# Kernel optimization log

Measured on AMD Instinct MI355X. Metric: run time of the kernel, lower is better.

## Reference

```python
import jax, jax.numpy as jnp
import numpy as np

D_MODEL = 1024
NUM_HEADS = 16
DEPTH = D_MODEL // NUM_HEADS
B, S = 2, 2048


def setup_inputs() -> dict:
    key = jax.random.key(0)
    k1, k2, k3 = jax.random.split(key, 3)
    x = jax.random.normal(k1, (B, S, D_MODEL), dtype=jnp.float32)
    # causal mask: 1.0 where attention is disallowed (upper triangle)
    causal = 1.0 - jnp.tril(jnp.ones((S, S), dtype=jnp.float32))
    mask = causal[None, None, :, :]  # [1,1,S,S]
    w_attn = jax.random.normal(k2, (D_MODEL, 3 * D_MODEL), dtype=jnp.float32) * 0.02
    b_attn = jnp.zeros((3 * D_MODEL,), dtype=jnp.float32)
    w_proj = jax.random.normal(k3, (D_MODEL, D_MODEL), dtype=jnp.float32) * 0.02
    b_proj = jnp.zeros((D_MODEL,), dtype=jnp.float32)
    return {"x": x, "mask": mask, "w_attn": w_attn, "b_attn": b_attn,
            "w_proj": w_proj, "b_proj": b_proj}


def _split_heads(t):
    # [B,S,D] -> [B,H,S,depth]
    b, s, _ = t.shape
    return t.reshape(b, s, NUM_HEADS, DEPTH).transpose(0, 2, 1, 3)


def reference(x, mask, w_attn, b_attn, w_proj, b_proj):
    # QKV projection (Conv1d == pointwise dense over last axis)
    qkv = jnp.einsum('bsd,de->bse', x, w_attn) + b_attn
    q, k, v = jnp.split(qkv, 3, axis=2)
    q, k, v = _split_heads(q), _split_heads(k), _split_heads(v)  # [B,H,S,depth]
    present = jnp.stack([k, v], axis=1)  # [B,2,H,S,depth]
    # scaled dot-product attention (inference: no dropout)
    scores = jnp.einsum('bhqd,bhkd->bhqk', q, k) / jnp.sqrt(
        jnp.asarray(DEPTH, dtype=x.dtype))
    scores = scores + mask * (-1e9)
    attn = jax.nn.softmax(scores, axis=-1)
    out = jnp.einsum('bhqk,bhkd->bhqd', attn, v)
    # merge heads: [B,H,S,depth] -> [B,S,D]
    out = out.transpose(0, 2, 1, 3).reshape(x.shape[0], -1, D_MODEL)
    out = jnp.einsum('bsd,de->bse', out, w_proj) + b_proj
    return out, present
```

## Files before the change

### kernel.cpp

```cpp
#include <hip/hip_runtime.h>
#include <stdint.h>

typedef unsigned short u16;
typedef unsigned int u32;
typedef short bf16x8 __attribute__((ext_vector_type(8)));
typedef float f32x4 __attribute__((ext_vector_type(4)));

#define SEQ 2048
#define NH 16
#define DM 1024
#define DEPTH 64

#define QSCALE 0.18033688f
#define SMAX 16.0f

__device__ __forceinline__ u16 f2bf(float f) {
  union { float f; u32 i; } v; v.f = f;
  u32 x = v.i;
  x += 0x7fffu + ((x >> 16) & 1u);
  return (u16)(x >> 16);
}

__device__ __forceinline__ float fexp2(float x) {
#if __has_builtin(__builtin_amdgcn_exp2f)
  return __builtin_amdgcn_exp2f(x);
#else
  return exp2f(x);
#endif
}

__device__ __forceinline__ void gload_lds16(const u16* g, u16* l) {
  __builtin_amdgcn_global_load_lds(
      (const __attribute__((address_space(1))) u32*)g,
      (__attribute__((address_space(3))) u32*)l, 16, 0, 0);
}

__global__ __launch_bounds__(256)
void cvt_bf16(const float* __restrict__ src, u16* __restrict__ dst) {
  int i = (blockIdx.x * 256 + threadIdx.x) * 4;
  float4 v = *(const float4*)(src + i);
  ushort4 o; o.x = f2bf(v.x); o.y = f2bf(v.y); o.z = f2bf(v.z); o.w = f2bf(v.w);
  *(ushort4*)(dst + i) = o;
}

__global__ __launch_bounds__(256)
void cvtT_both(const float* __restrict__ wa, const float* __restrict__ wp,
               u16* __restrict__ dwa, u16* __restrict__ dwp) {
  __shared__ float t[32][33];
  const int tid = threadIdx.x;
  const int bx = blockIdx.x;
  const float* src; u16* dst; int N, n0;
  if (bx < 96) { src = wa; dst = dwa; N = 3 * DM; n0 = bx << 5; }
  else         { src = wp; dst = dwp; N = DM;     n0 = (bx - 96) << 5; }
  const int k0 = blockIdx.y << 5;
  const int K = DM;
  {
    int r = tid >> 3, c4 = (tid & 7) << 2;
    float4 v = *(const float4*)(src + (size_t)(k0 + r) * N + n0 + c4);
    t[r][c4 + 0] = v.x; t[r][c4 + 1] = v.y; t[r][c4 + 2] = v.z; t[r][c4 + 3] = v.w;
  }
  __syncthreads();
  {
    int n = tid >> 3, k4 = (tid & 7) << 2;
    ushort4 o;
    o.x = f2bf(t[k4 + 0][n]); o.y = f2bf(t[k4 + 1][n]);
    o.z = f2bf(t[k4 + 2][n]); o.w = f2bf(t[k4 + 3][n]);
    *(ushort4*)(dst + (size_t)(n0 + n) * K + k0 + k4) = o;
  }
}

__global__ __launch_bounds__(256)
void v_transpose(const float* __restrict__ present, u16* __restrict__ vt) {
  __shared__ float t[64][65];
  const int tid = threadIdx.x;
  const int st = blockIdx.x, bh = blockIdx.y;
  const int b = bh >> 4, h = bh & 15;
  const int s0 = st << 6;
  const float* vsrc = present + (((size_t)((b * 2 + 1) * NH + h)) * SEQ + s0) * DEPTH;
  u16* vdst = vt + ((size_t)(b * NH + h) * DEPTH) * SEQ + s0;
#pragma unroll
  for (int i = 0; i < 4; ++i) {
    int e = tid + (i << 8);
    int r = e >> 4, c = e & 15;
    float4 v = *(const float4*)(vsrc + (size_t)r * DEPTH + (c << 2));
    t[r][(c << 2) + 0] = v.x; t[r][(c << 2) + 1] = v.y;
    t[r][(c << 2) + 2] = v.z; t[r][(c << 2) + 3] = v.w;
  }
  __syncthreads();
#pragma unroll
  for (int i = 0; i < 2; ++i) {
    int e = tid + (i << 8);
    int d = e >> 3, s8 = (e & 7) << 3;
    ushort4 o0, o1;
    o0.x = f2bf(t[s8 + 0][d]); o0.y = f2bf(t[s8 + 1][d]);
    o0.z = f2bf(t[s8 + 2][d]); o0.w = f2bf(t[s8 + 3][d]);
    o1.x = f2bf(t[s8 + 4][d]); o1.y = f2bf(t[s8 + 5][d]);
    o1.z = f2bf(t[s8 + 6][d]); o1.w = f2bf(t[s8 + 7][d]);
    *(ushort4*)(vdst + (size_t)d * SEQ + s8) = o0;
    *(ushort4*)(vdst + (size_t)d * SEQ + s8 + 4) = o1;
  }
}

__global__ __launch_bounds__(256)
void gemm_mfma(const u16* __restrict__ A, const u16* __restrict__ Bt,
               const float* __restrict__ bias, int M, int N, int K, int mode,
               float* __restrict__ outf, u16* __restrict__ qws,
               float* __restrict__ present, u16* __restrict__ kbp)
{
  __shared__ __align__(16) u16 As[128][64];
  __shared__ __align__(16) u16 Bs[128][64];
  const int tid = threadIdx.x;
  const int m0 = blockIdx.y << 7;
  const int n0 = blockIdx.x << 7;
  const int w = tid >> 6, lane = tid & 63;
  const int lane15 = lane & 15, quad = lane >> 4;
  const int wm = (w >> 1) << 6, wn = (w & 1) << 6;

  const int srow = lane >> 3;
  const int sseg = (lane & 7) ^ srow;
  const u16* agbase = A  + (size_t)(m0 + w * 32 + srow) * K + sseg * 8;
  const u16* bgbase = Bt + (size_t)(n0 + w * 32 + srow) * K + sseg * 8;

  const int l7 = lane15 & 7;

  f32x4 acc[4][4] = {};

  for (int k0 = 0; k0 < K; k0 += 64) {
#pragma unroll
    for (int i = 0; i < 4; ++i) {
      gload_lds16(agbase + (size_t)(i * 8) * K + k0, &As[w * 32 + i * 8][0]);
      gload_lds16(bgbase + (size_t)(i * 8) * K + k0, &Bs[w * 32 + i * 8][0]);
    }
    __syncthreads();
#pragma unroll
    for (int ks = 0; ks < 2; ++ks) {
      const int fs = ((ks * 4 + quad) ^ l7) << 3;
      bf16x8 af[4], bfr[4];
#pragma unroll
      for (int tm = 0; tm < 4; ++tm)
        af[tm] = *(const bf16x8*)&As[wm + tm * 16 + lane15][fs];
#pragma unroll
      for (int tn = 0; tn < 4; ++tn)
        bfr[tn] = *(const bf16x8*)&Bs[wn + tn * 16 + lane15][fs];
#pragma unroll
      for (int tm = 0; tm < 4; ++tm)
#pragma unroll
        for (int tn = 0; tn < 4; ++tn)
          acc[tm][tn] = __builtin_amdgcn_mfma_f32_16x16x32_bf16(af[tm], bfr[tn], acc[tm][tn], 0, 0, 0);
    }
    __syncthreads();
  }

#pragma unroll
  for (int tn = 0; tn < 4; ++tn) {
    const int c = n0 + wn + tn * 16 + lane15;
    const float bc = bias[c];
    const int t = c >> 10, cc = c & 1023;
    const int h = cc >> 6, d = cc & 63;
#pragma unroll
    for (int tm = 0; tm < 4; ++tm) {
#pragma unroll
      for (int r = 0; r < 4; ++r) {
        const int m = m0 + wm + tm * 16 + quad * 4 + r;
        const float val = acc[tm][tn][r] + bc;
        if (mode == 1) {
          outf[(size_t)m * N + c] = val;
        } else {
          const int b = m >> 11, s = m & 2047;
          if (t == 0) {
            qws[(((size_t)(b * NH + h) * SEQ) + s) * DEPTH + d] = f2bf(val * QSCALE);
          } else {
            const size_t pidx = (((size_t)((b * 2 + (t - 1)) * NH + h) * SEQ) + s) * DEPTH + d;
            present[pidx] = val;
            if (t == 1)
              kbp[(((size_t)(b * NH + h) * SEQ) + s) * DEPTH + d] = f2bf(val);
          }
        }
      }
    }
  }
}

__global__ __launch_bounds__(256)
void attn_mfma(const u16* __restrict__ qb, const u16* __restrict__ kb,
               const u16* __restrict__ vt, u16* __restrict__ attnb)
{
  __shared__ __align__(16) u16 Qs[64][72];
  __shared__ __align__(16) u16 Ks[64][72];
  __shared__ __align__(16) u16 VsT[64][72];
  __shared__ __align__(16) u16 Ps[64][72];

  const int tid = threadIdx.x;
  const int w = tid >> 6, lane = tid & 63;
  const int lane15 = lane & 15, quad = lane >> 4;
  const int p = blockIdx.x, bh = blockIdx.y;
  const int b = bh >> 4, h = bh & 15;

  const u16* qbh = qb + ((size_t)(b * NH + h) * SEQ) * DEPTH;
  const u16* kbh = kb + ((size_t)(b * NH + h) * SEQ) * DEPTH;
  const u16* vbh = vt + ((size_t)(b * NH + h) * DEPTH) * SEQ;

  bf16x8 ones;
#pragma unroll
  for (int j = 0; j < 8; ++j) ones[j] = (short)0x3F80;

  const int u0 = tid, u1 = tid + 256;
  u16* ksd0 = &Ks[u0 >> 3][(u0 & 7) << 3];
  u16* ksd1 = &Ks[u1 >> 3][(u1 & 7) << 3];
  u16* vsd0 = &VsT[u0 >> 3][(u0 & 7) << 3];
  u16* vsd1 = &VsT[u1 >> 3][(u1 & 7) << 3];
  const size_t voff0 = (size_t)(u0 >> 3) * SEQ + ((u0 & 7) << 3);
  const size_t voff1 = (size_t)(u1 >> 3) * SEQ + ((u1 & 7) << 3);

#pragma unroll 1
  for (int half = 0; half < 2; ++half) {
    const int tt = half ? (31 - p) : p;
    const int q0 = tt << 6;
    __syncthreads();
#pragma unroll
    for (int i = 0; i < 2; ++i) {
      int e = tid + (i << 8);
      *(bf16x8*)&Qs[e >> 3][(e & 7) << 3] =
          *(const bf16x8*)(qbh + (size_t)q0 * DEPTH + e * 8);
    }
    bf16x8 rk0 = *(const bf16x8*)(kbh + u0 * 8);
    bf16x8 rk1 = *(const bf16x8*)(kbh + u1 * 8);
    bf16x8 rv0 = *(const bf16x8*)(vbh + voff0);
    bf16x8 rv1 = *(const bf16x8*)(vbh + voff1);

    f32x4 accO[4] = {};
    f32x4 accL = {};
    const int qg = q0 + w * 16 + quad * 4;
    bf16x8 aQ0, aQ1;

    const int nchunk = tt + 1;
#pragma unroll 1
    for (int ct = 0; ct < nchunk; ++ct) {
      const int kk0 = ct << 6;
      __syncthreads();
      if (ct == 0) {
        aQ0 = *(const bf16x8*)&Qs[w * 16 + lane15][quad * 8];
        aQ1 = *(const bf16x8*)&Qs[w * 16 + lane15][32 + quad * 8];
      }
      *(bf16x8*)ksd0 = rk0; *(bf16x8*)ksd1 = rk1;
      *(bf16x8*)vsd0 = rv0; *(bf16x8*)vsd1 = rv1;
      __syncthreads();
      if (ct < tt) {
        const int kn = kk0 + 64;
        rk0 = *(const bf16x8*)(kbh + (size_t)kn * DEPTH + u0 * 8);
        rk1 = *(const bf16x8*)(kbh + (size_t)kn * DEPTH + u1 * 8);
        rv0 = *(const bf16x8*)(vbh + voff0 + kn);
        rv1 = *(const bf16x8*)(vbh + voff1 + kn);
      }
      f32x4 sc[4] = {};
#pragma unroll
      for (int tc = 0; tc < 4; ++tc) {
        bf16x8 bk0 = *(const bf16x8*)&Ks[tc * 16 + lane15][quad * 8];
        bf16x8 bk1 = *(const bf16x8*)&Ks[tc * 16 + lane15][32 + quad * 8];
        sc[tc] = __builtin_amdgcn_mfma_f32_16x16x32_bf16(aQ0, bk0, sc[tc], 0, 0, 0);
        sc[tc] = __builtin_amdgcn_mfma_f32_16x16x32_bf16(aQ1, bk1, sc[tc], 0, 0, 0);
      }
      const bool diag = (ct == tt);
#pragma unroll
      for (int tc = 0; tc < 4; ++tc) {
#pragma unroll
        for (int r = 0; r < 4; ++r) {
          float pe = fexp2(sc[tc][r] - SMAX);
          if (diag) {
            int kg = kk0 + tc * 16 + lane15;
            if (kg > qg + r) pe = 0.f;
          }
          Ps[w * 16 + quad * 4 + r][tc * 16 + lane15] = f2bf(pe);
        }
      }
#pragma unroll
      for (int ks = 0; ks < 2; ++ks) {
        bf16x8 ap = *(const bf16x8*)&Ps[w * 16 + lane15][ks * 32 + quad * 8];
        accL = __builtin_amdgcn_mfma_f32_16x16x32_bf16(ap, ones, accL, 0, 0, 0);
#pragma unroll
        for (int tn = 0; tn < 4; ++tn) {
          bf16x8 bv = *(const bf16x8*)&VsT[tn * 16 + lane15][ks * 32 + quad * 8];
          accO[tn] = __builtin_amdgcn_mfma_f32_16x16x32_bf16(ap, bv, accO[tn], 0, 0, 0);
        }
      }
    }

#pragma unroll
    for (int r = 0; r < 4; ++r) {
      const float li = 1.0f / accL[r];
      u16* obase = attnb + ((size_t)(b * SEQ + qg + r)) * DM + h * DEPTH;
#pragma unroll
      for (int tn = 0; tn < 4; ++tn)
        obase[tn * 16 + lane15] = f2bf(accO[tn][r] * li);
    }
  }
}

extern "C" void kernel_launch(void* const* d_in, const int* in_sizes, int n_in,
                              void* d_out, int out_size, void* d_ws, size_t ws_size,
                              hipStream_t stream) {
  (void)in_sizes; (void)n_in; (void)out_size; (void)ws_size;
  const float* x      = (const float*)d_in[0];
  const float* w_attn = (const float*)d_in[2];
  const float* b_attn = (const float*)d_in[3];
  const float* w_proj = (const float*)d_in[4];
  const float* b_proj = (const float*)d_in[5];

  float* out     = (float*)d_out;
  float* present = out + (size_t)2 * SEQ * DM;

  u16* qws   = (u16*)d_ws;
  u16* kbp   = qws + (size_t)4194304;
  u16* xb    = kbp + (size_t)4194304;
  u16* vtp   = xb;
  u16* wabT  = xb + (size_t)4194304;
  u16* attnb = wabT;
  u16* wpbT  = wabT + (size_t)4194304;

  cvt_bf16<<<4096, 256, 0, stream>>>(x, xb);
  cvtT_both<<<dim3(128, 32), 256, 0, stream>>>(w_attn, w_proj, wabT, wpbT);

  gemm_mfma<<<dim3(24, 32), 256, 0, stream>>>(xb, wabT, b_attn,
                                              2 * SEQ, 3 * DM, DM, 0,
                                              nullptr, qws, present, kbp);
  v_transpose<<<dim3(32, 32), 256, 0, stream>>>(present, vtp);
  attn_mfma<<<dim3(16, 32), 256, 0, stream>>>(qws, kbp, vtp, attnb);
  gemm_mfma<<<dim3(8, 32), 256, 0, stream>>>(attnb, wpbT, b_proj,
                                             2 * SEQ, DM, DM, 1,
                                             out, nullptr, nullptr, nullptr);
}
```

Measured before the change: 217.1 us.

## Rewrite attention kernel with 32x32 MFMA, register-resident P, and async double-buffered K/V

Restructures the causal attention kernel to use 32x32x16 MFMA tiles computing S^T with Q held in registers, so the probability tile feeds the PV MFMA directly from registers instead of round-tripping through LDS. K and V tiles are double-buffered in XOR-swizzled LDS via direct global-to-LDS loads, which overlaps the next chunk's fetch with compute and removes one barrier per chunk. Warps split the key dimension in halves, the row sum is accumulated in scalar registers rather than with a ones-MFMA, and partial outputs are reduced through LDS at the end. The wave whose diagonal sub-tile is fully masked skips it. The cost is an extra cross-warp reduction step and more register pressure from the 16-wide accumulators.

After: 225.6 us. +3.9%, slower.

```diff
diff --git a/kernel.cpp b/kernel.cpp
--- a/kernel.cpp
+++ b/kernel.cpp
@@ -5,6 +5,7 @@
 typedef unsigned int u32;
 typedef short bf16x8 __attribute__((ext_vector_type(8)));
 typedef float f32x4 __attribute__((ext_vector_type(4)));
+typedef float f32x16 __attribute__((ext_vector_type(16)));
 
 #define SEQ 2048
 #define NH 16
@@ -19,6 +20,10 @@
   u32 x = v.i;
   x += 0x7fffu + ((x >> 16) & 1u);
   return (u16)(x >> 16);
+}
+
+__device__ __forceinline__ float bf2f(u16 b) {
+  union { u32 i; float f; } u; u.i = ((u32)b) << 16; return u.f;
 }
 
 __device__ __forceinline__ float fexp2(float x) {
@@ -185,14 +190,13 @@
 void attn_mfma(const u16* __restrict__ qb, const u16* __restrict__ kb,
                const u16* __restrict__ vt, u16* __restrict__ attnb)
 {
-  __shared__ __align__(16) u16 Qs[64][72];
-  __shared__ __align__(16) u16 Ks[64][72];
-  __shared__ __align__(16) u16 VsT[64][72];
-  __shared__ __align__(16) u16 Ps[64][72];
+  __shared__ __align__(16) u16 Ks[2][64][64];
+  __shared__ __align__(16) u16 Vs[2][64][64];
 
   const int tid = threadIdx.x;
   const int w = tid >> 6, lane = tid & 63;
-  const int lane15 = lane & 15, quad = lane >> 4;
+  const int l31 = lane & 31, hi = lane >> 5;
+  const int qh = w >> 1, kh = w & 1;
   const int p = blockIdx.x, bh = blockIdx.y;
   const int b = bh >> 4, h = bh & 15;
 
@@ -200,98 +204,128 @@
   const u16* kbh = kb + ((size_t)(b * NH + h) * SEQ) * DEPTH;
   const u16* vbh = vt + ((size_t)(b * NH + h) * DEPTH) * SEQ;
 
-  bf16x8 ones;
-#pragma unroll
-  for (int j = 0; j < 8; ++j) ones[j] = (short)0x3F80;
-
-  const int u0 = tid, u1 = tid + 256;
-  u16* ksd0 = &Ks[u0 >> 3][(u0 & 7) << 3];
-  u16* ksd1 = &Ks[u1 >> 3][(u1 & 7) << 3];
-  u16* vsd0 = &VsT[u0 >> 3][(u0 & 7) << 3];
-  u16* vsd1 = &VsT[u1 >> 3][(u1 & 7) << 3];
-  const size_t voff0 = (size_t)(u0 >> 3) * SEQ + ((u0 & 7) << 3);
-  const size_t voff1 = (size_t)(u1 >> 3) * SEQ + ((u1 & 7) << 3);
+  const int srr = lane >> 3;
+  const int sseg = (lane & 7) ^ srr;
+  const int r0 = w * 16 + srr;
+  const int r1 = r0 + 8;
+  const int kr0 = (r0 & ~12) | ((r0 & 4) << 1) | ((r0 & 8) >> 1);
+  const int kr1 = (r1 & ~12) | ((r1 & 4) << 1) | ((r1 & 8) >> 1);
+
+  const int rbase = kh * 32 + l31;
+  const int swz = l31 & 7;
 
 #pragma unroll 1
   for (int half = 0; half < 2; ++half) {
     const int tt = half ? (31 - p) : p;
-    const int q0 = tt << 6;
-    __syncthreads();
-#pragma unroll
-    for (int i = 0; i < 2; ++i) {
-      int e = tid + (i << 8);
-      *(bf16x8*)&Qs[e >> 3][(e & 7) << 3] =
-          *(const bf16x8*)(qbh + (size_t)q0 * DEPTH + e * 8);
-    }
-    bf16x8 rk0 = *(const bf16x8*)(kbh + u0 * 8);
-    bf16x8 rk1 = *(const bf16x8*)(kbh + u1 * 8);
-    bf16x8 rv0 = *(const bf16x8*)(vbh + voff0);
-    bf16x8 rv1 = *(const bf16x8*)(vbh + voff1);
-
-    f32x4 accO[4] = {};
-    f32x4 accL = {};
-    const int qg = q0 + w * 16 + quad * 4;
-    bf16x8 aQ0, aQ1;
-
-    const int nchunk = tt + 1;
+    const int sloc = (tt << 6) + qh * 32 + l31;
+    __syncthreads();
+
+    gload_lds16(kbh + (size_t)kr0 * DEPTH + sseg * 8, &Ks[0][w * 16][0]);
+    gload_lds16(kbh + (size_t)kr1 * DEPTH + sseg * 8, &Ks[0][w * 16 + 8][0]);
+    gload_lds16(vbh + (size_t)r0 * SEQ + sseg * 8, &Vs[0][w * 16][0]);
+    gload_lds16(vbh + (size_t)r1 * SEQ + sseg * 8, &Vs[0][w * 16 + 8][0]);
+
+    const u16* qrow = qbh + (size_t)sloc * DEPTH + hi * 8;
+    bf16x8 qf0 = *(const bf16x8*)(qrow);
+    bf16x8 qf1 = *(const bf16x8*)(qrow + 16);
+    bf16x8 qf2 = *(const bf16x8*)(qrow + 32);
+    bf16x8 qf3 = *(const bf16x8*)(qrow + 48);
+
+    f32x16 accO0 = {};
+    f32x16 accO1 = {};
+    float L = 0.f;
+
+    const int nch = tt + 1;
+    __syncthreads();
 #pragma unroll 1
-    for (int ct = 0; ct < nchunk; ++ct) {
-      const int kk0 = ct << 6;
+    for (int ct = 0; ct < nch; ++ct) {
+      const int bb = ct & 1;
+      if (ct + 1 < nch) {
+        const int kn = (ct + 1) << 6;
+        gload_lds16(kbh + (size_t)(kn + kr0) * DEPTH + sseg * 8, &Ks[bb ^ 1][w * 16][0]);
+        gload_lds16(kbh + (size_t)(kn + kr1) * DEPTH + sseg * 8, &Ks[bb ^ 1][w * 16 + 8][0]);
+        gload_lds16(vbh + (size_t)r0 * SEQ + kn + sseg * 8, &Vs[bb ^ 1][w * 16][0]);
+        gload_lds16(vbh + (size_t)r1 * SEQ + kn + sseg * 8, &Vs[bb ^ 1][w * 16 + 8][0]);
+      }
+      const bool atdiag = (ct == tt);
+      if (!(atdiag && qh == 0 && kh == 1)) {
+        f32x16 sc;
+#pragma unroll
+        for (int j = 0; j < 16; ++j) sc[j] = -SMAX;
+        {
+          bf16x8 af0 = *(const bf16x8*)&Ks[bb][rbase][((0 + hi) ^ swz) * 8];
+          sc = __builtin_amdgcn_mfma_f32_32x32x16_bf16(af0, qf0, sc, 0, 0, 0);
+          bf16x8 af1 = *(const bf16x8*)&Ks[bb][rbase][((2 + hi) ^ swz) * 8];
+          sc = __builtin_amdgcn_mfma_f32_32x32x16_bf16(af1, qf1, sc, 0, 0, 0);
+          bf16x8 af2 = *(const bf16x8*)&Ks[bb][rbase][((4 + hi) ^ swz) * 8];
+          sc = __builtin_amdgcn_mfma_f32_32x32x16_bf16(af2, qf2, sc, 0, 0, 0);
+          bf16x8 af3 = *(const bf16x8*)&Ks[bb][rbase][((6 + hi) ^ swz) * 8];
+          sc = __builtin_amdgcn_mfma_f32_32x32x16_bf16(af3, qf3, sc, 0, 0, 0);
+        }
+        const bool dmask = atdiag && (qh == kh);
+        u16 pb[16];
+#pragma unroll
+        for (int j = 0; j < 16; ++j) {
+          float e = fexp2(sc[j]);
+          if (dmask) {
+            const int kg = (ct << 6) + kh * 32 + 16 * (j >> 3) + 8 * hi + (j & 7);
+            if (kg > sloc) e = 0.f;
+          }
+          const u16 pbj = f2bf(e);
+          pb[j] = pbj;
+          L += bf2f(pbj);
+        }
+        bf16x8 fr0, fr1;
+#pragma unroll
+        for (int j = 0; j < 8; ++j) { fr0[j] = (short)pb[j]; fr1[j] = (short)pb[8 + j]; }
+#pragma unroll
+        for (int s = 0; s < 2; ++s) {
+          const bf16x8 bp = s ? fr1 : fr0;
+          const int vcol = ((kh * 4 + 2 * s + hi) ^ swz) * 8;
+          bf16x8 av0 = *(const bf16x8*)&Vs[bb][l31][vcol];
+          accO0 = __builtin_amdgcn_mfma_f32_32x32x16_bf16(av0, bp, accO0, 0, 0, 0);
+          bf16x8 av1 = *(const bf16x8*)&Vs[bb][32 + l31][vcol];
+          accO1 = __builtin_amdgcn_mfma_f32_32x32x16_bf16(av1, bp, accO1, 0, 0, 0);
+        }
+      }
       __syncthreads();
-      if (ct == 0) {
-        aQ0 = *(const bf16x8*)&Qs[w * 16 + lane15][quad * 8];
-        aQ1 = *(const bf16x8*)&Qs[w * 16 + lane15][32 + quad * 8];
-      }
-      *(bf16x8*)ksd0 = rk0; *(bf16x8*)ksd1 = rk1;
-      *(bf16x8*)vsd0 = rv0; *(bf16x8*)vsd1 = rv1;
-      __syncthreads();
-      if (ct < tt) {
-        const int kn = kk0 + 64;
-        rk0 = *(const bf16x8*)(kbh + (size_t)kn * DEPTH + u0 * 8);
-        rk1 = *(const bf16x8*)(kbh + (size_t)kn * DEPTH + u1 * 8);
-        rv0 = *(const bf16x8*)(vbh + voff0 + kn);
-        rv1 = *(const bf16x8*)(vbh + voff1 + kn);
-      }
-      f32x4 sc[4] = {};
-#pragma unroll
-      for (int tc = 0; tc < 4; ++tc) {
-        bf16x8 bk0 = *(const bf16x8*)&Ks[tc * 16 + lane15][quad * 8];
-        bf16x8 bk1 = *(const bf16x8*)&Ks[tc * 16 + lane15][32 + quad * 8];
-        sc[tc] = __builtin_amdgcn_mfma_f32_16x16x32_bf16(aQ0, bk0, sc[tc], 0, 0, 0);
-        sc[tc] = __builtin_amdgcn_mfma_f32_16x16x32_bf16(aQ1, bk1, sc[tc], 0, 0, 0);
-      }
-      const bool diag = (ct == tt);
-#pragma unroll
-      for (int tc = 0; tc < 4; ++tc) {
-#pragma unroll
-        for (int r = 0; r < 4; ++r) {
-          float pe = fexp2(sc[tc][r] - SMAX);
-          if (diag) {
-            int kg = kk0 + tc * 16 + lane15;
-            if (kg > qg + r) pe = 0.f;
-          }
-          Ps[w * 16 + quad * 4 + r][tc * 16 + lane15] = f2bf(pe);
-        }
-      }
-#pragma unroll
-      for (int ks = 0; ks < 2; ++ks) {
-        bf16x8 ap = *(const bf16x8*)&Ps[w * 16 + lane15][ks * 32 + quad * 8];
-        accL = __builtin_amdgcn_mfma_f32_16x16x32_bf16(ap, ones, accL, 0, 0, 0);
-#pragma unroll
-        for (int tn = 0; tn < 4; ++tn) {
-          bf16x8 bv = *(const bf16x8*)&VsT[tn * 16 + lane15][ks * 32 + quad * 8];
-          accO[tn] = __builtin_amdgcn_mfma_f32_16x16x32_bf16(ap, bv, accO[tn], 0, 0, 0);
-        }
-      }
-    }
-
-#pragma unroll
-    for (int r = 0; r < 4; ++r) {
-      const float li = 1.0f / accL[r];
-      u16* obase = attnb + ((size_t)(b * SEQ + qg + r)) * DM + h * DEPTH;
-#pragma unroll
-      for (int tn = 0; tn < 4; ++tn)
-        obase[tn * 16 + lane15] = f2bf(accO[tn][r] * li);
+    }
+
+    float Lw = L + __shfl_xor(L, 32);
+    float* red  = (float*)&Ks[0][0][0];
+    float* redL = (float*)&Vs[0][0][0];
+    const int base = qh * 2048 + lane * 4;
+    if (kh) {
+#pragma unroll
+      for (int g = 0; g < 4; ++g) {
+        float4 v0 = make_float4(accO0[4 * g], accO0[4 * g + 1], accO0[4 * g + 2], accO0[4 * g + 3]);
+        *(float4*)&red[base + g * 256] = v0;
+        float4 v1 = make_float4(accO1[4 * g], accO1[4 * g + 1], accO1[4 * g + 2], accO1[4 * g + 3]);
+        *(float4*)&red[base + 1024 + g * 256] = v1;
+      }
+      redL[qh * 64 + lane] = Lw;
+    }
+    __syncthreads();
+    if (!kh) {
+      const float li = 1.0f / (Lw + redL[qh * 64 + lane]);
+      u16* ob = attnb + ((size_t)(b * SEQ + sloc)) * DM + h * DEPTH;
+#pragma unroll
+      for (int g = 0; g < 4; ++g) {
+        float4 p0 = *(const float4*)&red[base + g * 256];
+        ushort4 st0;
+        st0.x = f2bf((accO0[4 * g + 0] + p0.x) * li);
+        st0.y = f2bf((accO0[4 * g + 1] + p0.y) * li);
+        st0.z = f2bf((accO0[4 * g + 2] + p0.z) * li);
+        st0.w = f2bf((accO0[4 * g + 3] + p0.w) * li);
+        *(ushort4*)(ob + 8 * g + 4 * hi) = st0;
+        float4 p1 = *(const float4*)&red[base + 1024 + g * 256];
+        ushort4 st1;
+        st1.x = f2bf((accO1[4 * g + 0] + p1.x) * li);
+        st1.y = f2bf((accO1[4 * g + 1] + p1.y) * li);
+        st1.z = f2bf((accO1[4 * g + 2] + p1.z) * li);
+        st1.w = f2bf((accO1[4 * g + 3] + p1.w) * li);
+        *(ushort4*)(ob + 32 + 8 * g + 4 * hi) = st1;
+      }
     }
   }
 }
```
